# Performance work log

Hardware: AMD Instinct MI355X
Metric: run time of the kernel (lower is better)

## Reference

```python
import jax, jax.numpy as jnp
import numpy as np

HEADS = 12
DIM_HEAD = 64
SCALE = DIM_HEAD ** -0.5

def setup_inputs() -> dict:
    key = jax.random.key(0)
    k1, k2, k3, k4 = jax.random.split(key, 4)
    dim, inner = 768, HEADS * DIM_HEAD
    x = jax.random.normal(k1, (4, 2048, dim), dtype=jnp.float32)
    w_qkv = jax.random.normal(k2, (dim, 3 * inner), dtype=jnp.float32) * (dim ** -0.5)
    w_out = jax.random.normal(k3, (inner, dim), dtype=jnp.float32) * (inner ** -0.5)
    b_out = jax.random.normal(k4, (dim,), dtype=jnp.float32) * 0.02
    return {"x": x, "w_qkv": w_qkv, "w_out": w_out, "b_out": b_out}

def reference(x, w_qkv, w_out, b_out):
    B, N, _ = x.shape
    qkv = jnp.einsum('bnd,de->bne', x, w_qkv)  # [B,N,3*inner]
    q, k, v = jnp.split(qkv, 3, axis=-1)
    # b n (h d) -> b h n d
    split_heads = lambda t: t.reshape(B, N, HEADS, DIM_HEAD).transpose(0, 2, 1, 3)
    q, k, v = split_heads(q), split_heads(k), split_heads(v)
    dots = jnp.einsum('bhnd,bhmd->bhnm', q, k) * SCALE  # [B,H,N,N]
    attn = jax.nn.softmax(dots, axis=-1)
    out = jnp.einsum('bhnm,bhmd->bhnd', attn, v)
    out = out.transpose(0, 2, 1, 3).reshape(B, N, HEADS * DIM_HEAD)  # b h n d -> b n (h d)
    return jnp.einsum('bne,ed->bnd', out, w_out) + b_out
```

## Files before the change

### kernel.cpp

```cpp
#include <hip/hip_runtime.h>
#include <stdint.h>

typedef unsigned short ushort_t;
typedef __attribute__((ext_vector_type(8))) short short8;
typedef __attribute__((ext_vector_type(4))) short s16x4;
typedef __attribute__((ext_vector_type(4))) float f32x4;
typedef __attribute__((ext_vector_type(2))) uint32_t u32x2;

#define BATCH 4
#define SEQ 2048
#define DMODEL 768
#define NH 12
#define HD 64
#define QKV3 2304
#define NHEADS 48
#define SCALE_Q 0.18033688011112042f

__device__ __forceinline__ ushort_t f2bf(float f) {
    union { float f; uint32_t u; } v; v.f = f;
    uint32_t u = v.u;
    u += 0x7FFF + ((u >> 16) & 1);
    return (ushort_t)(u >> 16);
}

__device__ __forceinline__ uint32_t pack_bf16(float a, float b) {
#if __has_builtin(__builtin_amdgcn_cvt_pk_bf16_f32)
    typedef __attribute__((ext_vector_type(2))) __bf16 bf16x2;
    bf16x2 r = __builtin_amdgcn_cvt_pk_bf16_f32(a, b);
    return __builtin_bit_cast(uint32_t, r);
#else
    return ((uint32_t)f2bf(b) << 16) | (uint32_t)f2bf(a);
#endif
}

typedef __attribute__((address_space(1))) uint32_t as1_u32;
typedef __attribute__((address_space(3))) uint32_t as3_u32;
__device__ __forceinline__ void async16(void* lds, const void* gsrc) {
    __builtin_amdgcn_global_load_lds((as1_u32*)gsrc, (as3_u32*)lds, 16, 0, 0);
}

__device__ __forceinline__ void wait_vm_lgkm0() {
    __builtin_amdgcn_s_waitcnt(0x0070);
}

__device__ __forceinline__ f32x4 mfma16x16x16bf16(s16x4 a, s16x4 b, f32x4 c) {
#if __has_builtin(__builtin_amdgcn_mfma_f32_16x16x16bf16_1k)
    return __builtin_amdgcn_mfma_f32_16x16x16bf16_1k(a, b, c, 0, 0, 0);
#else
    f32x4 d;
    asm volatile("v_mfma_f32_16x16x16_bf16 %0, %1, %2, %3"
                 : "=&v"(d) : "v"(a), "v"(b), "0"(c));
    return d;
#endif
}

__global__ __launch_bounds__(256) void cvt_bf16(
    const float* __restrict__ in, ushort_t* __restrict__ out) {
    int i = blockIdx.x * 256 + threadIdx.x;
    float4 v = *(const float4*)(in + (size_t)i * 4);
    ushort4 o; o.x = f2bf(v.x); o.y = f2bf(v.y); o.z = f2bf(v.z); o.w = f2bf(v.w);
    *(ushort4*)(out + (size_t)i * 4) = o;
}

__global__ __launch_bounds__(256) void transpose_f32_bf16(
    const float* __restrict__ in, ushort_t* __restrict__ out, int R, int C) {
    __shared__ ushort_t t[64][72];
    const int tid = threadIdx.x;
    const int r0 = blockIdx.y * 64, c0 = blockIdx.x * 64;
#pragma unroll
    for (int i = 0; i < 4; i++) {
        int idx = tid + i * 256;
        int row = idx >> 4, c4 = (idx & 15) * 4;
        float4 v = *(const float4*)(in + (size_t)(r0 + row) * C + c0 + c4);
        ushort4 o; o.x = f2bf(v.x); o.y = f2bf(v.y); o.z = f2bf(v.z); o.w = f2bf(v.w);
        *(ushort4*)&t[row][c4] = o;
    }
    __syncthreads();
#pragma unroll
    for (int i = 0; i < 2; i++) {
        int idx = tid + i * 256;
        int oc = idx >> 3, g8 = (idx & 7) * 8;
        ushort_t tmp[8];
#pragma unroll
        for (int e = 0; e < 8; e++) tmp[e] = t[g8 + e][oc];
        *(short8*)(out + (size_t)(c0 + oc) * R + r0 + g8) = *(const short8*)tmp;
    }
}

__global__ __launch_bounds__(256) void transpose_v(
    const ushort_t* __restrict__ v, ushort_t* __restrict__ vt) {
    __shared__ ushort_t t[64][72];
    const int tid = threadIdx.x;
    const int head = blockIdx.y, n0 = blockIdx.x * 64;
    const ushort_t* src = v + (size_t)head * SEQ * HD + (size_t)n0 * HD;
#pragma unroll
    for (int i = 0; i < 2; i++) {
        int idx = tid + i * 256;
        int row = idx >> 3, c8 = (idx & 7) * 8;
        *(short8*)&t[row][c8] = *(const short8*)(src + (size_t)row * HD + c8);
    }
    __syncthreads();
    ushort_t* dst = vt + (size_t)head * HD * SEQ + n0;
#pragma unroll
    for (int i = 0; i < 2; i++) {
        int idx = tid + i * 256;
        int d = idx >> 3, g8 = (idx & 7) * 8;
        ushort_t tmp[8];
#pragma unroll
        for (int e = 0; e < 8; e++) tmp[e] = t[g8 + e][d];
        *(short8*)(dst + (size_t)d * SEQ + g8) = *(const short8*)tmp;
    }
}

__global__ __launch_bounds__(256, 2) void gemm_qkv(
    const ushort_t* __restrict__ A, const ushort_t* __restrict__ B,
    ushort_t* __restrict__ qkv) {
    __shared__ ushort_t As[128 * 64];
    __shared__ ushort_t Bs[128 * 64];

    const int tid = threadIdx.x;
    const int m0 = blockIdx.y * 128, n0 = blockIdx.x * 128;
    const int lane = tid & 63, w = tid >> 6;
    const int wm = w >> 1, wn = w & 1;
    const int l16 = lane & 15, quad = lane >> 4;

    f32x4 acc[4][4];
#pragma unroll
    for (int i = 0; i < 4; i++)
#pragma unroll
        for (int j = 0; j < 4; j++) acc[i][j] = (f32x4){0.f, 0.f, 0.f, 0.f};

    int srow[4], scol[4];
#pragma unroll
    for (int j = 0; j < 4; j++) {
        int s = j * 256 + tid;
        srow[j] = s >> 3;
        scol[j] = ((s & 7) ^ (srow[j] & 7)) * 8;
    }
    const int swz0 = (quad ^ (l16 & 7)) * 8;
    const int swz1 = ((4 + quad) ^ (l16 & 7)) * 8;

    for (int kt = 0; kt < DMODEL; kt += 64) {
#pragma unroll
        for (int j = 0; j < 4; j++) {
            async16(&As[(j * 256 + w * 64) * 8],
                    A + (size_t)(m0 + srow[j]) * DMODEL + kt + scol[j]);
            async16(&Bs[(j * 256 + w * 64) * 8],
                    B + (size_t)(n0 + srow[j]) * DMODEL + kt + scol[j]);
        }
        __syncthreads();

        short8 a[4][2], b[4][2];
#pragma unroll
        for (int mi = 0; mi < 4; mi++) {
            int r = (wm * 64 + mi * 16 + l16) * 64;
            a[mi][0] = *(const short8*)&As[r + swz0];
            a[mi][1] = *(const short8*)&As[r + swz1];
        }
#pragma unroll
        for (int ni = 0; ni < 4; ni++) {
            int r = (wn * 64 + ni * 16 + l16) * 64;
            b[ni][0] = *(const short8*)&Bs[r + swz0];
            b[ni][1] = *(const short8*)&Bs[r + swz1];
        }
#pragma unroll
        for (int kk = 0; kk < 2; kk++)
#pragma unroll
            for (int mi = 0; mi < 4; mi++)
#pragma unroll
                for (int ni = 0; ni < 4; ni++)
                    acc[mi][ni] = __builtin_amdgcn_mfma_f32_16x16x32_bf16(
                        a[mi][kk], b[ni][kk], acc[mi][ni], 0, 0, 0);
        __syncthreads();
    }

#pragma unroll
    for (int ni = 0; ni < 4; ni++) {
        int nbase = n0 + wn * 64 + ni * 16;
        int which = nbase / DMODEL;
        int rem = nbase - which * DMODEL;
        int h = rem >> 6;
        int d = (rem & 63) + l16;
        float scale = (which == 0) ? SCALE_Q : 1.0f;
#pragma unroll
        for (int mi = 0; mi < 4; mi++) {
#pragma unroll
            for (int r = 0; r < 4; r++) {
                int mg = m0 + wm * 64 + mi * 16 + quad * 4 + r;
                int b_ = mg >> 11, ns = mg & 2047;
                size_t dst = (((size_t)(which * BATCH + b_) * NH + h) * SEQ + ns) * HD + d;
                qkv[dst] = f2bf(acc[mi][ni][r] * scale);
            }
        }
    }
}

__global__ __launch_bounds__(256, 3) void attn(
    const ushort_t* __restrict__ qkv, const ushort_t* __restrict__ vT,
    ushort_t* __restrict__ ao) {
    __shared__ ushort_t smem[16384];

    const int tid = threadIdx.x;
    const int bh = blockIdx.x >> 4, qt = blockIdx.x & 15;
    const int lane = tid & 63, w = tid >> 6;
    const int l16 = lane & 15, quad = lane >> 4;
    const int qh7 = l16 & 7, qhi = quad >> 1, qlo4 = (quad & 1) * 4;

    const ushort_t* qh = qkv + (size_t)bh * (SEQ * HD);
    const ushort_t* kh = qkv + (size_t)(NHEADS + bh) * (SEQ * HD);
    const ushort_t* vh = vT + (size_t)bh * (HD * SEQ);

    short8 aq[2][2];
#pragma unroll
    for (int mi = 0; mi < 2; mi++)
#pragma unroll
        for (int kk = 0; kk < 2; kk++) {
            int row = qt * 128 + w * 32 + mi * 16 + l16;
            aq[mi][kk] = *(const short8*)(qh + (size_t)row * HD + kk * 32 + quad * 8);
        }

    f32x4 lv[2];
    f32x4 O[4][2];
#pragma unroll
    for (int mi = 0; mi < 2; mi++) lv[mi] = (f32x4){0.f, 0.f, 0.f, 0.f};
#pragma unroll
    for (int nd = 0; nd < 4; nd++)
#pragma unroll
        for (int mi = 0; mi < 2; mi++) O[nd][mi] = (f32x4){0.f, 0.f, 0.f, 0.f};

    int srow[2], scol[2];
#pragma unroll
    for (int j = 0; j < 2; j++) {
        int s = j * 256 + tid;
        srow[j] = s >> 3;
        scol[j] = ((s & 7) ^ (srow[j] & 7)) * 8;
    }
    const int swz0 = (quad ^ qh7) * 8;
    const int swz1 = ((4 + quad) ^ qh7) * 8;

#pragma unroll
    for (int j = 0; j < 2; j++) {
        async16(&smem[(j * 256 + w * 64) * 8],
                kh + (size_t)srow[j] * HD + scol[j]);
        async16(&smem[4096 + (j * 256 + w * 64) * 8],
                vh + (size_t)srow[j] * SEQ + scol[j]);
    }

    const int NT = SEQ / 64;
    for (int t = 0; t < NT; t++) {
        wait_vm_lgkm0();
        __syncthreads();
        if (t + 1 < NT) {
            int nb = ((t + 1) & 1) * 8192, j1 = (t + 1) * 64;
#pragma unroll
            for (int j = 0; j < 2; j++) {
                async16(&smem[nb + (j * 256 + w * 64) * 8],
                        kh + (size_t)(j1 + srow[j]) * HD + scol[j]);
                async16(&smem[nb + 4096 + (j * 256 + w * 64) * 8],
                        vh + (size_t)srow[j] * SEQ + j1 + scol[j]);
            }
        }
        const ushort_t* Ks = smem + (t & 1) * 8192;
        const ushort_t* Vs = Ks + 4096;

        f32x4 S[4][2];
#pragma unroll
        for (int ni = 0; ni < 4; ni++)
#pragma unroll
            for (int mi = 0; mi < 2; mi++) S[ni][mi] = (f32x4){0.f, 0.f, 0.f, 0.f};
        short8 ak[4][2];
#pragma unroll
        for (int ni = 0; ni < 4; ni++) {
            int r = (ni * 16 + l16) * 64;
            ak[ni][0] = *(const short8*)&Ks[r + swz0];
            ak[ni][1] = *(const short8*)&Ks[r + swz1];
        }
#pragma unroll
        for (int kk = 0; kk < 2; kk++)
#pragma unroll
            for (int ni = 0; ni < 4; ni++)
#pragma unroll
                for (int mi = 0; mi < 2; mi++)
                    S[ni][mi] = __builtin_amdgcn_mfma_f32_16x16x32_bf16(
                        ak[ni][kk], aq[mi][kk], S[ni][mi], 0, 0, 0);

#pragma unroll
        for (int mi = 0; mi < 2; mi++)
#pragma unroll
            for (int ni = 0; ni < 4; ni++) {
                f32x4 p;
#pragma unroll
                for (int r = 0; r < 4; r++)
                    p[r] = __builtin_amdgcn_exp2f(S[ni][mi][r]);
                S[ni][mi] = p;
                lv[mi] += p;
            }

#pragma unroll
        for (int kb = 0; kb < 4; kb++) {
            s16x4 bp[2];
#pragma unroll
            for (int mi = 0; mi < 2; mi++) {
                uint32_t lo = pack_bf16(S[kb][mi][0], S[kb][mi][1]);
                uint32_t hi = pack_bf16(S[kb][mi][2], S[kb][mi][3]);
                bp[mi] = __builtin_bit_cast(s16x4, (u32x2){lo, hi});
            }
#pragma unroll
            for (int nd = 0; nd < 4; nd++) {
                int vrow = nd * 16 + l16;
                s16x4 av = *(const s16x4*)&Vs[vrow * 64 +
                                              (((kb * 2 + qhi) ^ qh7) * 8) + qlo4];
#pragma unroll
                for (int mi = 0; mi < 2; mi++)
                    O[nd][mi] = mfma16x16x16bf16(av, bp[mi], O[nd][mi]);
            }
        }
    }

    float inv[2];
#pragma unroll
    for (int mi = 0; mi < 2; mi++) {
        float l = (lv[mi][0] + lv[mi][1]) + (lv[mi][2] + lv[mi][3]);
        l += __shfl_xor(l, 16, 64);
        l += __shfl_xor(l, 32, 64);
        inv[mi] = __builtin_amdgcn_rcpf(l);
    }
    wait_vm_lgkm0();
    __syncthreads();
    ushort_t* Lt = smem;
#pragma unroll
    for (int mi = 0; mi < 2; mi++)
#pragma unroll
        for (int nd = 0; nd < 4; nd++) {
            int row = w * 32 + mi * 16 + l16;
            int col = nd * 16 + quad * 4;
            uint32_t d0 = pack_bf16(O[nd][mi][0] * inv[mi], O[nd][mi][1] * inv[mi]);
            uint32_t d1 = pack_bf16(O[nd][mi][2] * inv[mi], O[nd][mi][3] * inv[mi]);
            *(u32x2*)&Lt[row * 72 + col] = (u32x2){d0, d1};
        }
    __syncthreads();

    const int b_ = bh / NH, h = bh % NH;
#pragma unroll
    for (int i = 0; i < 4; i++) {
        int idx = tid + i * 256;
        int row = idx >> 3, c8 = (idx & 7) * 8;
        short8 vv = *(const short8*)&Lt[row * 72 + c8];
        *(short8*)(ao + ((size_t)(b_ * SEQ + qt * 128 + row)) * DMODEL +
                   h * HD + c8) = vv;
    }
}

__global__ __launch_bounds__(256, 2) void gemm_out(
    const ushort_t* __restrict__ A, const ushort_t* __restrict__ B,
    const float* __restrict__ bias, float* __restrict__ out) {
    __shared__ ushort_t As[128 * 64];
    __shared__ ushort_t Bs[128 * 64];

    const int tid = threadIdx.x;
    const int m0 = blockIdx.y * 128, n0 = blockIdx.x * 128;
    const int lane = tid & 63, w = tid >> 6;
    const int wm = w >> 1, wn = w & 1;
    const int l16 = lane & 15, quad = lane >> 4;

    f32x4 acc[4][4];
#pragma unroll
    for (int i = 0; i < 4; i++)
#pragma unroll
        for (int j = 0; j < 4; j++) acc[i][j] = (f32x4){0.f, 0.f, 0.f, 0.f};

    int srow[4], scol[4];
#pragma unroll
    for (int j = 0; j < 4; j++) {
        int s = j * 256 + tid;
        srow[j] = s >> 3;
        scol[j] = ((s & 7) ^ (srow[j] & 7)) * 8;
    }
    const int swz0 = (quad ^ (l16 & 7)) * 8;
    const int swz1 = ((4 + quad) ^ (l16 & 7)) * 8;

    for (int kt = 0; kt < DMODEL; kt += 64) {
#pragma unroll
        for (int j = 0; j < 4; j++) {
            async16(&As[(j * 256 + w * 64) * 8],
                    A + (size_t)(m0 + srow[j]) * DMODEL + kt + scol[j]);
            async16(&Bs[(j * 256 + w * 64) * 8],
                    B + (size_t)(n0 + srow[j]) * DMODEL + kt + scol[j]);
        }
        __syncthreads();

        short8 a[4][2], b[4][2];
#pragma unroll
        for (int mi = 0; mi < 4; mi++) {
            int r = (wm * 64 + mi * 16 + l16) * 64;
            a[mi][0] = *(const short8*)&As[r + swz0];
            a[mi][1] = *(const short8*)&As[r + swz1];
        }
#pragma unroll
        for (int ni = 0; ni < 4; ni++) {
            int r = (wn * 64 + ni * 16 + l16) * 64;
            b[ni][0] = *(const short8*)&Bs[r + swz0];
            b[ni][1] = *(const short8*)&Bs[r + swz1];
        }
#pragma unroll
        for (int kk = 0; kk < 2; kk++)
#pragma unroll
            for (int mi = 0; mi < 4; mi++)
#pragma unroll
                for (int ni = 0; ni < 4; ni++)
                    acc[mi][ni] = __builtin_amdgcn_mfma_f32_16x16x32_bf16(
                        a[mi][kk], b[ni][kk], acc[mi][ni], 0, 0, 0);
        __syncthreads();
    }

#pragma unroll
    for (int ni = 0; ni < 4; ni++) {
        int ng = n0 + wn * 64 + ni * 16 + l16;
        float bv = bias[ng];
#pragma unroll
        for (int mi = 0; mi < 4; mi++) {
#pragma unroll
            for (int r = 0; r < 4; r++) {
                int mg = m0 + wm * 64 + mi * 16 + quad * 4 + r;
                out[(size_t)mg * DMODEL + ng] = acc[mi][ni][r] + bv;
            }
        }
    }
}

extern "C" void kernel_launch(void* const* d_in, const int* in_sizes, int n_in,
                              void* d_out, int out_size, void* d_ws, size_t ws_size,
                              hipStream_t stream) {
    const float* x     = (const float*)d_in[0];
    const float* w_qkv = (const float*)d_in[1];
    const float* w_out = (const float*)d_in[2];
    const float* b_out = (const float*)d_in[3];
    float* out = (float*)d_out;

    ushort_t* xb  = (ushort_t*)d_ws;
    ushort_t* wqT = xb  + (size_t)8192 * 768;
    ushort_t* woT = wqT + (size_t)QKV3 * 768;
    ushort_t* qkv = woT + (size_t)768 * 768;
    ushort_t* vT  = qkv + (size_t)3 * NHEADS * SEQ * HD;
    ushort_t* ao  = vT  + (size_t)NHEADS * HD * SEQ;

    cvt_bf16<<<dim3((8192 * 768) / 4 / 256), 256, 0, stream>>>(x, xb);
    transpose_f32_bf16<<<dim3(QKV3 / 64, DMODEL / 64), 256, 0, stream>>>(
        w_qkv, wqT, DMODEL, QKV3);
    transpose_f32_bf16<<<dim3(DMODEL / 64, DMODEL / 64), 256, 0, stream>>>(
        w_out, woT, DMODEL, DMODEL);

    gemm_qkv<<<dim3(QKV3 / 128, (BATCH * SEQ) / 128), 256, 0, stream>>>(xb, wqT, qkv);

    transpose_v<<<dim3(SEQ / 64, NHEADS), 256, 0, stream>>>(
        qkv + (size_t)2 * NHEADS * SEQ * HD, vT);

    attn<<<dim3(NHEADS * (SEQ / 128)), 256, 0, stream>>>(qkv, vT, ao);

    gemm_out<<<dim3(DMODEL / 128, (BATCH * SEQ) / 128), 256, 0, stream>>>(
        ao, woT, b_out, out);
}
```

Baseline: 228.4 us.

## Fuse V transpose into QKV GEMM epilogue, interleave attention S/PV, remap blocks

The QKV GEMM epilogue now writes V directly in transposed layout using packed 4-element stores, which removes the separate transpose_v kernel and its extra global round trip. The attention inner loop computes S, exp2 and the PV MFMA one 16-key slice at a time instead of materializing all S tiles first, which lowers register pressure. Attention blocks are reordered so that consecutive blocks cover different heads. Explicit vm/lgkm waits are added before the barriers in both GEMMs, and these appear to fix a missing async-load wait.

```diff
diff --git a/kernel.cpp b/kernel.cpp
--- a/kernel.cpp
+++ b/kernel.cpp
@@ -87,34 +87,9 @@
     }
 }
 
-__global__ __launch_bounds__(256) void transpose_v(
-    const ushort_t* __restrict__ v, ushort_t* __restrict__ vt) {
-    __shared__ ushort_t t[64][72];
-    const int tid = threadIdx.x;
-    const int head = blockIdx.y, n0 = blockIdx.x * 64;
-    const ushort_t* src = v + (size_t)head * SEQ * HD + (size_t)n0 * HD;
-#pragma unroll
-    for (int i = 0; i < 2; i++) {
-        int idx = tid + i * 256;
-        int row = idx >> 3, c8 = (idx & 7) * 8;
-        *(short8*)&t[row][c8] = *(const short8*)(src + (size_t)row * HD + c8);
-    }
-    __syncthreads();
-    ushort_t* dst = vt + (size_t)head * HD * SEQ + n0;
-#pragma unroll
-    for (int i = 0; i < 2; i++) {
-        int idx = tid + i * 256;
-        int d = idx >> 3, g8 = (idx & 7) * 8;
-        ushort_t tmp[8];
-#pragma unroll
-        for (int e = 0; e < 8; e++) tmp[e] = t[g8 + e][d];
-        *(short8*)(dst + (size_t)d * SEQ + g8) = *(const short8*)tmp;
-    }
-}
-
 __global__ __launch_bounds__(256, 2) void gemm_qkv(
     const ushort_t* __restrict__ A, const ushort_t* __restrict__ B,
-    ushort_t* __restrict__ qkv) {
+    ushort_t* __restrict__ qkv, ushort_t* __restrict__ vT) {
     __shared__ ushort_t As[128 * 64];
     __shared__ ushort_t Bs[128 * 64];
 
@@ -148,6 +123,7 @@
             async16(&Bs[(j * 256 + w * 64) * 8],
                     B + (size_t)(n0 + srow[j]) * DMODEL + kt + scol[j]);
         }
+        wait_vm_lgkm0();
         __syncthreads();
 
         short8 a[4][2], b[4][2];
@@ -181,15 +157,26 @@
         int rem = nbase - which * DMODEL;
         int h = rem >> 6;
         int d = (rem & 63) + l16;
-        float scale = (which == 0) ? SCALE_Q : 1.0f;
-#pragma unroll
-        for (int mi = 0; mi < 4; mi++) {
-#pragma unroll
-            for (int r = 0; r < 4; r++) {
-                int mg = m0 + wm * 64 + mi * 16 + quad * 4 + r;
+        if (which == 2) {
+#pragma unroll
+            for (int mi = 0; mi < 4; mi++) {
+                int mg = m0 + wm * 64 + mi * 16 + quad * 4;
                 int b_ = mg >> 11, ns = mg & 2047;
-                size_t dst = (((size_t)(which * BATCH + b_) * NH + h) * SEQ + ns) * HD + d;
-                qkv[dst] = f2bf(acc[mi][ni][r] * scale);
+                u32x2 pk = {pack_bf16(acc[mi][ni][0], acc[mi][ni][1]),
+                            pack_bf16(acc[mi][ni][2], acc[mi][ni][3])};
+                *(u32x2*)(vT + ((size_t)(b_ * NH + h) * HD + d) * SEQ + ns) = pk;
+            }
+        } else {
+            float scale = (which == 0) ? SCALE_Q : 1.0f;
+#pragma unroll
+            for (int mi = 0; mi < 4; mi++) {
+#pragma unroll
+                for (int r = 0; r < 4; r++) {
+                    int mg = m0 + wm * 64 + mi * 16 + quad * 4 + r;
+                    int b_ = mg >> 11, ns = mg & 2047;
+                    size_t dst = (((size_t)(which * BATCH + b_) * NH + h) * SEQ + ns) * HD + d;
+                    qkv[dst] = f2bf(acc[mi][ni][r] * scale);
+                }
             }
         }
     }
@@ -201,7 +188,10 @@
     __shared__ ushort_t smem[16384];
 
     const int tid = threadIdx.x;
-    const int bh = blockIdx.x >> 4, qt = blockIdx.x & 15;
+    const int bid = blockIdx.x;
+    const int i = bid >> 3;
+    const int bh = (bid & 7) + 8 * (i % 6);
+    const int qt = i / 6;
     const int lane = tid & 63, w = tid >> 6;
     const int l16 = lane & 15, quad = lane >> 4;
     const int qh7 = l16 & 7, qhi = quad >> 1, qlo4 = (quad & 1) * 4;
@@ -263,53 +253,31 @@
         const ushort_t* Ks = smem + (t & 1) * 8192;
         const ushort_t* Vs = Ks + 4096;
 
-        f32x4 S[4][2];
-#pragma unroll
-        for (int ni = 0; ni < 4; ni++)
-#pragma unroll
-            for (int mi = 0; mi < 2; mi++) S[ni][mi] = (f32x4){0.f, 0.f, 0.f, 0.f};
-        short8 ak[4][2];
 #pragma unroll
         for (int ni = 0; ni < 4; ni++) {
             int r = (ni * 16 + l16) * 64;
-            ak[ni][0] = *(const short8*)&Ks[r + swz0];
-            ak[ni][1] = *(const short8*)&Ks[r + swz1];
-        }
-#pragma unroll
-        for (int kk = 0; kk < 2; kk++)
-#pragma unroll
-            for (int ni = 0; ni < 4; ni++)
-#pragma unroll
-                for (int mi = 0; mi < 2; mi++)
-                    S[ni][mi] = __builtin_amdgcn_mfma_f32_16x16x32_bf16(
-                        ak[ni][kk], aq[mi][kk], S[ni][mi], 0, 0, 0);
-
-#pragma unroll
-        for (int mi = 0; mi < 2; mi++)
-#pragma unroll
-            for (int ni = 0; ni < 4; ni++) {
+            short8 ak0 = *(const short8*)&Ks[r + swz0];
+            short8 ak1 = *(const short8*)&Ks[r + swz1];
+            s16x4 bp[2];
+#pragma unroll
+            for (int mi = 0; mi < 2; mi++) {
+                f32x4 s = __builtin_amdgcn_mfma_f32_16x16x32_bf16(
+                    ak0, aq[mi][0], (f32x4){0.f, 0.f, 0.f, 0.f}, 0, 0, 0);
+                s = __builtin_amdgcn_mfma_f32_16x16x32_bf16(
+                    ak1, aq[mi][1], s, 0, 0, 0);
                 f32x4 p;
 #pragma unroll
-                for (int r = 0; r < 4; r++)
-                    p[r] = __builtin_amdgcn_exp2f(S[ni][mi][r]);
-                S[ni][mi] = p;
+                for (int rr = 0; rr < 4; rr++)
+                    p[rr] = __builtin_amdgcn_exp2f(s[rr]);
                 lv[mi] += p;
-            }
-
-#pragma unroll
-        for (int kb = 0; kb < 4; kb++) {
-            s16x4 bp[2];
-#pragma unroll
-            for (int mi = 0; mi < 2; mi++) {
-                uint32_t lo = pack_bf16(S[kb][mi][0], S[kb][mi][1]);
-                uint32_t hi = pack_bf16(S[kb][mi][2], S[kb][mi][3]);
-                bp[mi] = __builtin_bit_cast(s16x4, (u32x2){lo, hi});
+                bp[mi] = __builtin_bit_cast(
+                    s16x4, (u32x2){pack_bf16(p[0], p[1]), pack_bf16(p[2], p[3])});
             }
 #pragma unroll
             for (int nd = 0; nd < 4; nd++) {
                 int vrow = nd * 16 + l16;
                 s16x4 av = *(const s16x4*)&Vs[vrow * 64 +
-                                              (((kb * 2 + qhi) ^ qh7) * 8) + qlo4];
+                                              (((ni * 2 + qhi) ^ qh7) * 8) + qlo4];
 #pragma unroll
                 for (int mi = 0; mi < 2; mi++)
                     O[nd][mi] = mfma16x16x16bf16(av, bp[mi], O[nd][mi]);
@@ -342,8 +310,8 @@
 
     const int b_ = bh / NH, h = bh % NH;
 #pragma unroll
-    for (int i = 0; i < 4; i++) {
-        int idx = tid + i * 256;
+    for (int i2 = 0; i2 < 4; i2++) {
+        int idx = tid + i2 * 256;
         int row = idx >> 3, c8 = (idx & 7) * 8;
         short8 vv = *(const short8*)&Lt[row * 72 + c8];
         *(short8*)(ao + ((size_t)(b_ * SEQ + qt * 128 + row)) * DMODEL +
@@ -387,6 +355,7 @@
             async16(&Bs[(j * 256 + w * 64) * 8],
                     B + (size_t)(n0 + srow[j]) * DMODEL + kt + scol[j]);
         }
+        wait_vm_lgkm0();
         __syncthreads();
 
         short8 a[4][2], b[4][2];
@@ -450,10 +419,8 @@
     transpose_f32_bf16<<<dim3(DMODEL / 64, DMODEL / 64), 256, 0, stream>>>(
         w_out, woT, DMODEL, DMODEL);
 
-    gemm_qkv<<<dim3(QKV3 / 128, (BATCH * SEQ) / 128), 256, 0, stream>>>(xb, wqT, qkv);
-
-    transpose_v<<<dim3(SEQ / 64, NHEADS), 256, 0, stream>>>(
-        qkv + (size_t)2 * NHEADS * SEQ * HD, vT);
+    gemm_qkv<<<dim3(QKV3 / 128, (BATCH * SEQ) / 128), 256, 0, stream>>>(
+        xb, wqT, qkv, vT);
 
     attn<<<dim3(NHEADS * (SEQ / 128)), 256, 0, stream>>>(qkv, vT, ao);
 
```

After: 218.5 us. 1.04x faster.
